# Kernel optimization log

Measured on AMD Instinct MI355X. Metric: run time of the kernel, lower is better.

## Reference

```python
import jax, jax.numpy as jnp
import numpy as np

E = 131072   # total messages
N = 8192     # dim_size (num nodes)
D = 256      # input_dim == hidden_dim (forced by h + m add)


def setup_inputs() -> dict:
    key = jax.random.key(0)
    k1, k2, k3, k4, k5 = jax.random.split(key, 5)
    msg = jax.random.normal(k1, (E, D), dtype=jnp.float32)
    index = jax.random.randint(k2, (E,), 0, N)
    t = jax.random.uniform(k3, (E,), dtype=jnp.float32)
    # torch.nn.Linear(D, D) params (kaiming-uniform-ish scale)
    W = jax.random.normal(k4, (D, D), dtype=jnp.float32) / np.sqrt(D)
    b = (jax.random.normal(k5, (D,), dtype=jnp.float32) * 0.01)
    return {"msg": msg, "index": index, "t": t, "dim_size": N, "W": W, "b": b}


def reference(msg, index, t, dim_size, W, b):
    # Original: for each node, sort its messages by t, then run the linear
    # recurrence h <- W @ (m + h) + b starting from h = 0; nodes with no
    # messages keep h = 0. Vectorized: one global stable sort by (index, t),
    # then a single segmented lax.scan with reset at segment boundaries.
    num_msgs, d = msg.shape
    order = jnp.lexsort((t, index))          # primary key: index, secondary: t
    m_sorted = msg[order]                     # [E, d]
    seg = index[order]                        # [E]

    def step(carry, inp):
        h, prev = carry
        m, s = inp
        h_in = jnp.where(s == prev, h, jnp.zeros_like(h))  # reset at new segment
        h_new = (m + h_in) @ W.T + b
        return (h_new, s), h_new

    init = (jnp.zeros((d,), msg.dtype), jnp.asarray(-1, seg.dtype))
    _, ys = jax.lax.scan(step, init, (m_sorted, seg))      # ys: [E, d]

    # final hidden per node = h at the last message of its segment
    pos = jnp.arange(num_msgs)
    last = jax.ops.segment_max(pos, seg, num_segments=dim_size)
    counts = jax.ops.segment_sum(jnp.ones((num_msgs,), jnp.int32), seg,
                                 num_segments=dim_size)
    gathered = ys[jnp.clip(last, 0, num_msgs - 1)]          # [N, d]
    hidden = jnp.where((counts > 0)[:, None], gathered, jnp.zeros_like(gathered))
    return hidden
```

## Files before the change

### kernel.cpp

```cpp
#include <hip/hip_runtime.h>
#include <hip/hip_bf16.h>

#define E_MSGS 131072
#define N_NODES 8192
#define D_DIM 256
#define XA_STRIDE 264

typedef __bf16 bf16x8 __attribute__((ext_vector_type(8)));
typedef float f32x4 __attribute__((ext_vector_type(4)));

typedef const __attribute__((address_space(1))) void cg_void;
typedef __attribute__((address_space(3))) void lds_void;


__global__ void k_count(const int* __restrict__ index, int* __restrict__ counts) {
    int e = blockIdx.x * blockDim.x + threadIdx.x;
    if (e < E_MSGS) atomicAdd(&counts[index[e]], 1);
}

__global__ void k_prep(const int* __restrict__ counts, int* __restrict__ offsets,
                       int* __restrict__ perm) {
    __shared__ int partial[256];
    __shared__ int hist[256];
    __shared__ int hscan[256];
    __shared__ int hcur[256];
    int tid = threadIdx.x;
    hist[tid] = 0;
    __syncthreads();

    int base = tid * 32;
    int local[32];
    int sum = 0;
#pragma unroll
    for (int i = 0; i < 32; i++) {
        local[i] = sum;
        int c = counts[base + i];
        sum += c;
        atomicAdd(&hist[min(c, 255)], 1);
    }
    partial[tid] = sum;
    __syncthreads();
    for (int off = 1; off < 256; off <<= 1) {
        int v = (tid >= off) ? partial[tid - off] : 0;
        __syncthreads();
        partial[tid] += v;
        __syncthreads();
    }
    int basesum = (tid > 0) ? partial[tid - 1] : 0;
#pragma unroll
    for (int i = 0; i < 32; i++) offsets[base + i] = basesum + local[i];
    if (tid == 255) offsets[N_NODES] = partial[255];

    hscan[tid] = hist[255 - tid];
    __syncthreads();
    for (int off = 1; off < 256; off <<= 1) {
        int v = (tid >= off) ? hscan[tid - off] : 0;
        __syncthreads();
        hscan[tid] += v;
        __syncthreads();
    }
    hcur[tid] = hscan[255 - tid] - hist[tid];
    __syncthreads();
#pragma unroll
    for (int i = 0; i < 32; i++) {
        int n = base + i;
        int c = min(counts[n], 255);
        int pos = atomicAdd(&hcur[c], 1);
        perm[pos] = n;
    }
}

__global__ void k_scatter(const int* __restrict__ index, const int* __restrict__ offsets,
                          int* __restrict__ cursors, int* __restrict__ bucket) {
    int e = blockIdx.x * blockDim.x + threadIdx.x;
    if (e < E_MSGS) {
        int n = index[e];
        int p = offsets[n] + atomicAdd(&cursors[n], 1);
        bucket[p] = e;
    }
}

__global__ void k_rank(const int* __restrict__ index, const float* __restrict__ t,
                       const int* __restrict__ offsets, const int* __restrict__ bucket,
                       int* __restrict__ sorted_id) {
    int p = blockIdx.x * blockDim.x + threadIdx.x;
    if (p < E_MSGS) {
        int e = bucket[p];
        int n = index[e];
        int beg = offsets[n], end = offsets[n + 1];
        float te = t[e];
        int r = 0;
        for (int q = beg; q < end; q++) {
            int e2 = bucket[q];
            float t2 = t[e2];
            r += (t2 < te) || (t2 == te && e2 < e);
        }
        sorted_id[beg + r] = e;
    }
}


__launch_bounds__(256, 2)
__global__ void k_gru(const float* __restrict__ msg, const float* __restrict__ W,
                      const float* __restrict__ b, const int* __restrict__ offsets,
                      const int* __restrict__ sorted_id, const int* __restrict__ perm,
                      float* __restrict__ out) {
    __shared__ __bf16 xA[2][16 * XA_STRIDE];
    __shared__ float msg_lds[2][16][D_DIM];

    int tid  = threadIdx.x;
    int wave = tid >> 6;
    int lane = tid & 63;
    int q    = lane >> 4;
    int l    = lane & 15;
    int node0 = blockIdx.x * 16;

    bf16x8 wf[8][4];
#pragma unroll
    for (int t4 = 0; t4 < 4; t4++) {
        const float* wr = W + (64 * wave + 16 * t4 + l) * D_DIM;
#pragma unroll
        for (int c = 0; c < 8; c++) {
            int k0 = 32 * c + 8 * q;
            float4 w0 = *(const float4*)(wr + k0);
            float4 w1 = *(const float4*)(wr + k0 + 4);
            bf16x8 f;
            f[0] = (__bf16)w0.x; f[1] = (__bf16)w0.y; f[2] = (__bf16)w0.z; f[3] = (__bf16)w0.w;
            f[4] = (__bf16)w1.x; f[5] = (__bf16)w1.y; f[6] = (__bf16)w1.z; f[7] = (__bf16)w1.w;
            wf[c][t4] = f;
        }
    }
    float bias[4];
#pragma unroll
    for (int t4 = 0; t4 < 4; t4++) bias[t4] = b[64 * wave + 16 * t4 + l];

    int nodeC[4], off4[4], cnt4[4];
#pragma unroll
    for (int r = 0; r < 4; r++) {
        int n = perm[node0 + 4 * q + r];
        nodeC[r] = n;
        int o0 = offsets[n], o1 = offsets[n + 1];
        off4[r] = o0; cnt4[r] = o1 - o0;
    }
    int S = 0;
    for (int i = 0; i < 16; i++) {
        int n = perm[node0 + i];
        S = max(S, offsets[n + 1] - offsets[n]);
    }

    int offG[4];
#pragma unroll
    for (int j = 0; j < 4; j++) offG[j] = offsets[perm[node0 + 4 * wave + j]];

#pragma unroll
    for (int j = 0; j < 4; j++) {
        int sid0 = sorted_id[min(offG[j], E_MSGS - 1)];
        int sid1 = sorted_id[min(offG[j] + 1, E_MSGS - 1)];
        const float* g0 = msg + (long)sid0 * D_DIM + 4 * lane;
        const float* g1 = msg + (long)sid1 * D_DIM + 4 * lane;
        float* l0 = &msg_lds[0][4 * wave + j][4 * lane];
        float* l1 = &msg_lds[1][4 * wave + j][4 * lane];
        __builtin_amdgcn_global_load_lds((cg_void*)g0, (lds_void*)l0, 16, 0, 0);
        __builtin_amdgcn_global_load_lds((cg_void*)g1, (lds_void*)l1, 16, 0, 0);
    }
    int sidg[4];
#pragma unroll
    for (int j = 0; j < 4; j++) sidg[j] = sorted_id[min(offG[j] + 2, E_MSGS - 1)];
    __syncthreads();

    {
        int row = tid >> 4;
        int c0  = tid & 15;
#pragma unroll
        for (int k = 0; k < 16; k++) {
            int col = c0 + 16 * k;
            xA[0][row * XA_STRIDE + col] = (__bf16)msg_lds[0][row][col];
        }
    }

    float h[4][4];
#pragma unroll
    for (int t4 = 0; t4 < 4; t4++)
#pragma unroll
        for (int r = 0; r < 4; r++) h[t4][r] = 0.f;
    __syncthreads();

    for (int s = 0; s < S; s++) {
#pragma unroll
        for (int j = 0; j < 4; j++) {
            const float* g = msg + (long)sidg[j] * D_DIM + 4 * lane;
            float* ld = &msg_lds[s & 1][4 * wave + j][4 * lane];
            __builtin_amdgcn_global_load_lds((cg_void*)g, (lds_void*)ld, 16, 0, 0);
        }
#pragma unroll
        for (int j = 0; j < 4; j++)
            sidg[j] = sorted_id[min(offG[j] + s + 3, E_MSGS - 1)];

        const __bf16* buf = xA[s & 1];
        f32x4 acc[4];
#pragma unroll
        for (int t4 = 0; t4 < 4; t4++) acc[t4] = (f32x4){0.f, 0.f, 0.f, 0.f};
#pragma unroll
        for (int c = 0; c < 8; c++) {
            bf16x8 a = *(const bf16x8*)(buf + l * XA_STRIDE + 32 * c + 8 * q);
#pragma unroll
            for (int t4 = 0; t4 < 4; t4++)
                acc[t4] = __builtin_amdgcn_mfma_f32_16x16x32_bf16(a, wf[c][t4], acc[t4], 0, 0, 0);
        }

        __bf16* nbuf = xA[(s + 1) & 1];
        const float (*mbuf)[D_DIM] = msg_lds[(s + 1) & 1];
#pragma unroll
        for (int t4 = 0; t4 < 4; t4++) {
#pragma unroll
            for (int r = 0; r < 4; r++) {
                float hn = acc[t4][r] + bias[t4];
                bool valid = s < cnt4[r];
                h[t4][r] = valid ? hn : h[t4][r];
                float mv = mbuf[4 * q + r][64 * wave + 16 * t4 + l];
                nbuf[(4 * q + r) * XA_STRIDE + 64 * wave + 16 * t4 + l] =
                    (__bf16)(h[t4][r] + mv);
            }
        }
        __syncthreads();
    }

#pragma unroll
    for (int t4 = 0; t4 < 4; t4++)
#pragma unroll
        for (int r = 0; r < 4; r++)
            out[(long)nodeC[r] * D_DIM + 64 * wave + 16 * t4 + l] = h[t4][r];
}


extern "C" void kernel_launch(void* const* d_in, const int* in_sizes, int n_in,
                              void* d_out, int out_size, void* d_ws, size_t ws_size,
                              hipStream_t stream) {
    const float* msg   = (const float*)d_in[0];
    const int*   index = (const int*)d_in[1];
    const float* t     = (const float*)d_in[2];
    const float* W     = (const float*)d_in[4];
    const float* b     = (const float*)d_in[5];
    float* out = (float*)d_out;

    int* ws = (int*)d_ws;
    int* counts    = ws;
    int* cursors   = ws + 8192;
    int* offsets   = ws + 16384;
    int* perm      = ws + 24584;
    int* bucket    = ws + 32776;
    int* sorted_id = ws + 163848;

    hipMemsetAsync(counts, 0, 16384 * sizeof(int), stream);
    k_count<<<E_MSGS / 256, 256, 0, stream>>>(index, counts);
    k_prep<<<1, 256, 0, stream>>>(counts, offsets, perm);
    k_scatter<<<E_MSGS / 256, 256, 0, stream>>>(index, offsets, cursors, bucket);
    k_rank<<<E_MSGS / 256, 256, 0, stream>>>(index, t, offsets, bucket, sorted_id);
    k_gru<<<N_NODES / 16, 256, 0, stream>>>(msg, W, b, offsets, sorted_id, perm, out);
}
```

Measured before the change: 262.4 us.

## Sort segments with wave shuffles and load messages directly to registers in GRU

Replaces the per-element global-memory ranking with a one-wave-per-node rank sort using shuffles, which assumes at most 64 messages per node. The GRU kernel drops the LDS message staging and prefetches next-step message values straight into registers with double buffering. The max-segment loop is replaced by reading the first node of the count-sorted perm, and barriers are lightened to wait only on LDS counters. The register prefetch raises register pressure and issues uncoalesced per-lane scalar loads.

```diff
diff --git a/kernel.cpp b/kernel.cpp
--- a/kernel.cpp
+++ b/kernel.cpp
@@ -9,8 +9,7 @@
 typedef __bf16 bf16x8 __attribute__((ext_vector_type(8)));
 typedef float f32x4 __attribute__((ext_vector_type(4)));
 
-typedef const __attribute__((address_space(1))) void cg_void;
-typedef __attribute__((address_space(3))) void lds_void;
+#define BAR() asm volatile("s_waitcnt lgkmcnt(0)\n\ts_barrier" ::: "memory")
 
 
 __global__ void k_count(const int* __restrict__ index, int* __restrict__ counts) {
@@ -80,23 +79,21 @@
     }
 }
 
-__global__ void k_rank(const int* __restrict__ index, const float* __restrict__ t,
-                       const int* __restrict__ offsets, const int* __restrict__ bucket,
-                       int* __restrict__ sorted_id) {
-    int p = blockIdx.x * blockDim.x + threadIdx.x;
-    if (p < E_MSGS) {
-        int e = bucket[p];
-        int n = index[e];
-        int beg = offsets[n], end = offsets[n + 1];
-        float te = t[e];
-        int r = 0;
-        for (int q = beg; q < end; q++) {
-            int e2 = bucket[q];
-            float t2 = t[e2];
-            r += (t2 < te) || (t2 == te && e2 < e);
-        }
-        sorted_id[beg + r] = e;
-    }
+__global__ void k_sortseg(const float* __restrict__ t, const int* __restrict__ offsets,
+                          const int* __restrict__ bucket, int* __restrict__ sorted_id) {
+    int wid = (blockIdx.x * 256 + threadIdx.x) >> 6;
+    int ln = threadIdx.x & 63;
+    int beg = offsets[wid], end = offsets[wid + 1];
+    int cnt = end - beg;
+    int e = 0; float tv = 0.f;
+    if (ln < cnt) { e = bucket[beg + ln]; tv = t[e]; }
+    int rank = 0;
+    for (int j = 0; j < cnt; j++) {
+        float tj = __shfl(tv, j);
+        int ej = __shfl(e, j);
+        rank += (tj < tv) || (tj == tv && ej < e);
+    }
+    if (ln < cnt) sorted_id[beg + rank] = e;
 }
 
 
@@ -106,7 +103,6 @@
                       const int* __restrict__ sorted_id, const int* __restrict__ perm,
                       float* __restrict__ out) {
     __shared__ __bf16 xA[2][16 * XA_STRIDE];
-    __shared__ float msg_lds[2][16][D_DIM];
 
     int tid  = threadIdx.x;
     int wave = tid >> 6;
@@ -139,62 +135,46 @@
     for (int r = 0; r < 4; r++) {
         int n = perm[node0 + 4 * q + r];
         nodeC[r] = n;
-        int o0 = offsets[n], o1 = offsets[n + 1];
-        off4[r] = o0; cnt4[r] = o1 - o0;
-    }
-    int S = 0;
-    for (int i = 0; i < 16; i++) {
-        int n = perm[node0 + i];
-        S = max(S, offsets[n + 1] - offsets[n]);
-    }
-
-    int offG[4];
-#pragma unroll
-    for (int j = 0; j < 4; j++) offG[j] = offsets[perm[node0 + 4 * wave + j]];
-
-#pragma unroll
-    for (int j = 0; j < 4; j++) {
-        int sid0 = sorted_id[min(offG[j], E_MSGS - 1)];
-        int sid1 = sorted_id[min(offG[j] + 1, E_MSGS - 1)];
-        const float* g0 = msg + (long)sid0 * D_DIM + 4 * lane;
-        const float* g1 = msg + (long)sid1 * D_DIM + 4 * lane;
-        float* l0 = &msg_lds[0][4 * wave + j][4 * lane];
-        float* l1 = &msg_lds[1][4 * wave + j][4 * lane];
-        __builtin_amdgcn_global_load_lds((cg_void*)g0, (lds_void*)l0, 16, 0, 0);
-        __builtin_amdgcn_global_load_lds((cg_void*)g1, (lds_void*)l1, 16, 0, 0);
-    }
-    int sidg[4];
-#pragma unroll
-    for (int j = 0; j < 4; j++) sidg[j] = sorted_id[min(offG[j] + 2, E_MSGS - 1)];
-    __syncthreads();
-
-    {
-        int row = tid >> 4;
-        int c0  = tid & 15;
-#pragma unroll
-        for (int k = 0; k < 16; k++) {
-            int col = c0 + 16 * k;
-            xA[0][row * XA_STRIDE + col] = (__bf16)msg_lds[0][row][col];
-        }
-    }
+        off4[r] = offsets[n];
+        cnt4[r] = offsets[n + 1] - off4[r];
+    }
+    int nfirst = perm[node0];
+    int S = offsets[nfirst + 1] - offsets[nfirst];
 
     float h[4][4];
 #pragma unroll
     for (int t4 = 0; t4 < 4; t4++)
 #pragma unroll
         for (int r = 0; r < 4; r++) h[t4][r] = 0.f;
-    __syncthreads();
-
-    for (int s = 0; s < S; s++) {
-#pragma unroll
-        for (int j = 0; j < 4; j++) {
-            const float* g = msg + (long)sidg[j] * D_DIM + 4 * lane;
-            float* ld = &msg_lds[s & 1][4 * wave + j][4 * lane];
-            __builtin_amdgcn_global_load_lds((cg_void*)g, (lds_void*)ld, 16, 0, 0);
-        }
-#pragma unroll
-        for (int j = 0; j < 4; j++)
-            sidg[j] = sorted_id[min(offG[j] + s + 3, E_MSGS - 1)];
+
+    float mvA[4][4], mvB[4][4];
+    int sidp[4];
+#pragma unroll
+    for (int r = 0; r < 4; r++) {
+        int sid0 = sorted_id[min(off4[r], E_MSGS - 1)];
+        int sid1 = sorted_id[min(off4[r] + 1, E_MSGS - 1)];
+        const float* m0 = msg + (long)sid0 * D_DIM;
+        const float* m1 = msg + (long)sid1 * D_DIM;
+#pragma unroll
+        for (int t4 = 0; t4 < 4; t4++) {
+            int col = 64 * wave + 16 * t4 + l;
+            xA[0][(4 * q + r) * XA_STRIDE + col] = (__bf16)m0[col];
+            mvA[r][t4] = m1[col];
+        }
+        sidp[r] = sorted_id[min(off4[r] + 2, E_MSGS - 1)];
+    }
+    BAR();
+
+    auto step = [&](int s, float (&cur)[4][4], float (&nxt)[4][4]) {
+#pragma unroll
+        for (int r = 0; r < 4; r++) {
+            const float* mrow = msg + (long)sidp[r] * D_DIM;
+#pragma unroll
+            for (int t4 = 0; t4 < 4; t4++) nxt[r][t4] = mrow[64 * wave + 16 * t4 + l];
+        }
+#pragma unroll
+        for (int r = 0; r < 4; r++)
+            sidp[r] = sorted_id[min(off4[r] + s + 3, E_MSGS - 1)];
 
         const __bf16* buf = xA[s & 1];
         f32x4 acc[4];
@@ -209,7 +189,6 @@
         }
 
         __bf16* nbuf = xA[(s + 1) & 1];
-        const float (*mbuf)[D_DIM] = msg_lds[(s + 1) & 1];
 #pragma unroll
         for (int t4 = 0; t4 < 4; t4++) {
 #pragma unroll
@@ -217,12 +196,20 @@
                 float hn = acc[t4][r] + bias[t4];
                 bool valid = s < cnt4[r];
                 h[t4][r] = valid ? hn : h[t4][r];
-                float mv = mbuf[4 * q + r][64 * wave + 16 * t4 + l];
                 nbuf[(4 * q + r) * XA_STRIDE + 64 * wave + 16 * t4 + l] =
-                    (__bf16)(h[t4][r] + mv);
+                    (__bf16)(h[t4][r] + cur[r][t4]);
             }
         }
-        __syncthreads();
+        BAR();
+    };
+
+    int s = 0;
+    while (s < S) {
+        step(s, mvA, mvB);
+        s++;
+        if (s >= S) break;
+        step(s, mvB, mvA);
+        s++;
     }
 
 #pragma unroll
@@ -252,9 +239,10 @@
     int* sorted_id = ws + 163848;
 
     hipMemsetAsync(counts, 0, 16384 * sizeof(int), stream);
+
     k_count<<<E_MSGS / 256, 256, 0, stream>>>(index, counts);
     k_prep<<<1, 256, 0, stream>>>(counts, offsets, perm);
     k_scatter<<<E_MSGS / 256, 256, 0, stream>>>(index, offsets, cursors, bucket);
-    k_rank<<<E_MSGS / 256, 256, 0, stream>>>(index, t, offsets, bucket, sorted_id);
+    k_sortseg<<<N_NODES * 64 / 256, 256, 0, stream>>>(t, offsets, bucket, sorted_id);
     k_gru<<<N_NODES / 16, 256, 0, stream>>>(msg, W, b, offsets, sorted_id, perm, out);
 }
```

Result: faster. 256.4 us (-2.3%).
